# Kernel tuning notes

Hardware: AMD Instinct MI355X
Metric: run time of the kernel (lower is better)

Reference implementation:

```python
import math
import jax, jax.numpy as jnp
import numpy as np
from jax import lax

B = 4; N = 4096; F = 15; A = 24          # batch, tcr_num, feature_num, aa_num
HID = 10; H = 1; HD = 10; AFN = 14       # attn hidden, heads, head dim, sum(filter_num)
KS = [2, 3, 4, 5, 6, 7]; FN = [3, 3, 3, 2, 2, 1]
K = int(N * 0.05)                        # routing topk = 204
SCALE = np.float32(1.0 / math.sqrt(HD))


def setup_inputs() -> dict:
    key = jax.random.key(0)
    ks = jax.random.split(key, 24)
    inp = {"x": jax.random.normal(ks[0], (B, N, F, A), jnp.float32)}
    for i, (h, f) in enumerate(zip(KS, FN)):
        inp["conv_w%d" % h] = jax.random.normal(ks[1 + 2 * i], (f, F, h), jnp.float32) * 0.1
        inp["conv_b%d" % h] = jax.random.normal(ks[2 + 2 * i], (f,), jnp.float32) * 0.1
    specs = [("q", HID, AFN), ("k", HID, AFN), ("v", HID, AFN), ("attn", AFN, HID), ("mil", 2, AFN)]
    for j, (nm, o, i_) in enumerate(specs):
        inp["w_" + nm] = jax.random.normal(ks[13 + 2 * j], (o, i_), jnp.float32) * 0.1
        inp["b_" + nm] = jax.random.normal(ks[14 + 2 * j], (o,), jnp.float32) * 0.1
    return inp


def reference(x, conv_w2, conv_b2, conv_w3, conv_b3, conv_w4, conv_b4,
              conv_w5, conv_b5, conv_w6, conv_b6, conv_w7, conv_b7,
              w_q, b_q, w_k, b_k, w_v, b_v, w_attn, b_attn, w_mil, b_mil):
    # --- per-sequence conv feature extraction ---
    xc = x.reshape(-1, F, A)  # [B*N, 15, 24]
    feats = []
    for w, b in [(conv_w2, conv_b2), (conv_w3, conv_b3), (conv_w4, conv_b4),
                 (conv_w5, conv_b5), (conv_w6, conv_b6), (conv_w7, conv_b7)]:
        y = lax.conv_general_dilated(xc, w, (1,), 'VALID',
                                     dimension_numbers=('NCH', 'OIH', 'NCH'))
        y = jax.nn.relu(y + b[None, :, None])
        feats.append(jnp.max(y, axis=-1))  # AdaptiveMaxPool1d(1)
    out = jnp.concatenate(feats, axis=1).reshape(B, N, AFN)  # [B, N, 14]

    # --- QKV projections, split into heads -> [B, H, N, HD] ---
    q = (out @ w_q.T + b_q).reshape(B, N, H, HD).transpose(0, 2, 1, 3)
    k = (out @ w_k.T + b_k).reshape(B, N, H, HD).transpose(0, 2, 1, 3)
    v = (out @ w_v.T + b_v).reshape(B, N, H, HD).transpose(0, 2, 1, 3)

    # --- bi-level routing: full scores, topk over head-mean (detached in torch) ---
    scores_raw = jnp.einsum('bhnd,bhmd->bhnm', q, k)  # [B, H, N, N]
    a_r = jnp.mean(lax.stop_gradient(scores_raw), axis=1)  # [B, N, N]
    _, idx = lax.top_k(a_r, K)  # [B, N, K] int32
    idx_r = jnp.broadcast_to(idx[:, None], (B, H, N, K))

    scores = jnp.take_along_axis(scores_raw * SCALE, idx_r, axis=3)  # [B, H, N, K]
    # gather values per (batch, head, query): v_g[b,h,i,j] = v[b,h,idx[b,h,i,j]]
    v_g = jax.vmap(jax.vmap(lambda vh, ih: vh[ih]))(v, idx_r)  # [B, H, N, K, HD]

    probs = jax.nn.softmax(scores, axis=-1)  # dropout is identity at p=0 / eval
    ctx = jnp.einsum('bhnk,bhnkd->bhnd', probs, v_g)  # [B, H, N, HD]
    ctx = ctx.transpose(0, 2, 1, 3).reshape(B, N, HID)

    ctx = ctx @ w_attn.T + b_attn          # [B, N, 14]
    logits = ctx @ w_mil.T + b_mil          # [B, N, 2]
    pooled = jnp.sum(logits, axis=1) / N    # [B, 2]
    return pooled, probs[:, :, :, None, :]  # probs shaped [B, H, N, 1, K] as in torch
```

## Files before the change

### kernel.cpp

```cpp
#include <hip/hip_runtime.h>
#include <math.h>

#define NB 4
#define NN 4096
#define KSEL 204
#define NBINS 512
#define CANDN 256
#define QKSCALE 0.31622776601683794f

#define WS_Q 0
#define WS_KT (NB * NN * 10)
#define WS_V (2 * NB * NN * 10)
#define WS_LG (3 * NB * NN * 10)

#define SEQ_PER_BLOCK 16

__global__ __launch_bounds__(256) void featqkv_kernel(
    const float* __restrict__ x,
    const float* __restrict__ w2, const float* __restrict__ b2,
    const float* __restrict__ w3, const float* __restrict__ b3,
    const float* __restrict__ w4, const float* __restrict__ b4,
    const float* __restrict__ w5, const float* __restrict__ b5,
    const float* __restrict__ w6, const float* __restrict__ b6,
    const float* __restrict__ w7, const float* __restrict__ b7,
    const float* __restrict__ wq, const float* __restrict__ bq,
    const float* __restrict__ wk, const float* __restrict__ bk,
    const float* __restrict__ wv, const float* __restrict__ bv,
    float* __restrict__ q_out, float* __restrict__ kT_out, float* __restrict__ v_out)
{
    __shared__ float xs[SEQ_PER_BLOCK * 360];
    __shared__ float wconv[840];
    __shared__ float bconv[14];
    __shared__ float wqkv[420];
    __shared__ float bqkv[30];
    __shared__ float feats[SEQ_PER_BLOCK * 14];

    const int t = threadIdx.x;
    const int g0 = blockIdx.x * SEQ_PER_BLOCK;

    const float* xg = x + (size_t)g0 * 360;
    for (int i = t; i < SEQ_PER_BLOCK * 360; i += 256) xs[i] = xg[i];
    for (int i = t; i < 90; i += 256) wconv[i] = w2[i];
    for (int i = t; i < 135; i += 256) wconv[90 + i] = w3[i];
    for (int i = t; i < 180; i += 256) wconv[225 + i] = w4[i];
    for (int i = t; i < 150; i += 256) wconv[405 + i] = w5[i];
    for (int i = t; i < 180; i += 256) wconv[555 + i] = w6[i];
    for (int i = t; i < 105; i += 256) wconv[735 + i] = w7[i];
    if (t < 3) bconv[t] = b2[t];
    else if (t < 6) bconv[t] = b3[t - 3];
    else if (t < 9) bconv[t] = b4[t - 6];
    else if (t < 11) bconv[t] = b5[t - 9];
    else if (t < 13) bconv[t] = b6[t - 11];
    else if (t == 13) bconv[t] = b7[0];
    for (int i = t; i < 140; i += 256) wqkv[i] = wq[i];
    for (int i = t; i < 140; i += 256) wqkv[140 + i] = wk[i];
    for (int i = t; i < 140; i += 256) wqkv[280 + i] = wv[i];
    if (t < 10) bqkv[t] = bq[t];
    else if (t < 20) bqkv[t] = bk[t - 10];
    else if (t < 30) bqkv[t] = bv[t - 20];
    __syncthreads();

    const int seq = t >> 4;
    const int wkr = t & 15;

    if (wkr < 14) {
        const int ch = wkr;
        int h, fi, woff;
        if (ch < 3)       { h = 2; fi = ch;      woff = 0   + fi * 30; }
        else if (ch < 6)  { h = 3; fi = ch - 3;  woff = 90  + fi * 45; }
        else if (ch < 9)  { h = 4; fi = ch - 6;  woff = 225 + fi * 60; }
        else if (ch < 11) { h = 5; fi = ch - 9;  woff = 405 + fi * 75; }
        else if (ch < 13) { h = 6; fi = ch - 11; woff = 555 + fi * 90; }
        else              { h = 7; fi = 0;       woff = 735; }
        const int T = 24 - h + 1;

        float acc[23];
#pragma unroll
        for (int i2 = 0; i2 < 23; i2++) acc[i2] = 0.f;
        const float* xrow = &xs[seq * 360];
        for (int c = 0; c < 15; c++) {
            float xr[24];
#pragma unroll
            for (int u = 0; u < 24; u++) xr[u] = xrow[c * 24 + u];
#pragma unroll
            for (int j = 0; j < 7; j++) {
                if (j < h) {
                    float wv_ = wconv[woff + c * h + j];
#pragma unroll
                    for (int tt = 0; tt < 23; tt++) {
                        if (tt < T) acc[tt] = fmaf(xr[tt + j], wv_, acc[tt]);
                    }
                }
            }
        }
        float m = -1e30f;
#pragma unroll
        for (int tt = 0; tt < 23; tt++) {
            if (tt < T) m = fmaxf(m, acc[tt]);
        }
        feats[seq * 14 + ch] = fmaxf(m + bconv[ch], 0.f);
    }
    __syncthreads();

    const int g = g0 + seq;
    const int b_ = g >> 12;
    const int n_ = g & 4095;
    for (int o = wkr; o < 30; o += 16) {
        const int type = o / 10;
        const int comp = o % 10;
        const float* wrow = &wqkv[type * 140 + comp * 14];
        const float* frow = &feats[seq * 14];
        float a = bqkv[type * 10 + comp];
#pragma unroll
        for (int ii = 0; ii < 14; ii++) a = fmaf(frow[ii], wrow[ii], a);
        if (type == 0) q_out[(size_t)g * 10 + comp] = a;
        else if (type == 1) kT_out[((size_t)b_ * 10 + comp) * NN + n_] = a;
        else v_out[(size_t)g * 10 + comp] = a;
    }
}

__device__ __forceinline__ float dec_key(unsigned int k) {
    return (k & 0x80000000u) ? __uint_as_float(k ^ 0x80000000u)
                             : __uint_as_float(~k);
}
__device__ __forceinline__ unsigned int enc_key(float s) {
    unsigned int u = __float_as_uint(s);
    return (u & 0x80000000u) ? ~u : (u | 0x80000000u);
}

__global__ __launch_bounds__(256, 6) void attn_kernel(
    const float* __restrict__ qbuf, const float* __restrict__ kTbuf,
    const float* __restrict__ vbuf,
    const float* __restrict__ w_attn, const float* __restrict__ b_attn,
    const float* __restrict__ w_mil, const float* __restrict__ b_mil,
    float* __restrict__ out_probs, float* __restrict__ logits)
{
    __shared__ unsigned int base_[NBINS];
    __shared__ unsigned int bc_[NBINS];
    __shared__ unsigned long long cand[CANDN];
    __shared__ float hpart[4], lpart[4], fpart[4];
    __shared__ unsigned int wtot[4];
    __shared__ float ctxp[40];
    __shared__ float ctx_sh[10];
    __shared__ float attn_sh[14];

    const int t = threadIdx.x;
    const int lane = t & 63;
    const int w = t >> 6;
    const int row = blockIdx.x;
    const int b_ = row >> 12;

    float q0, q1, q2, q3, q4, q5, q6, q7, q8, q9;
    {
        const float* qp = qbuf + (size_t)row * 10;
        q0 = qp[0]; q1 = qp[1]; q2 = qp[2]; q3 = qp[3]; q4 = qp[4];
        q5 = qp[5]; q6 = qp[6]; q7 = qp[7]; q8 = qp[8]; q9 = qp[9];
    }
    const float* kTb = kTbuf + (size_t)b_ * 10 * NN;
    float sc[16];
    float vhi = -1e30f, vlo = 1e30f;
#pragma unroll
    for (int i = 0; i < 4; i++) {
        float4 a0 = make_float4(0.f, 0.f, 0.f, 0.f);
#pragma unroll
        for (int c = 0; c < 10; c++) {
            const float qc = (c == 0) ? q0 : (c == 1) ? q1 : (c == 2) ? q2 : (c == 3) ? q3 :
                             (c == 4) ? q4 : (c == 5) ? q5 : (c == 6) ? q6 : (c == 7) ? q7 :
                             (c == 8) ? q8 : q9;
            const float4 kv = reinterpret_cast<const float4*>(kTb + c * NN)[i * 256 + t];
            a0.x = fmaf(qc, kv.x, a0.x);
            a0.y = fmaf(qc, kv.y, a0.y);
            a0.z = fmaf(qc, kv.z, a0.z);
            a0.w = fmaf(qc, kv.w, a0.w);
        }
        sc[i * 4 + 0] = a0.x; sc[i * 4 + 1] = a0.y;
        sc[i * 4 + 2] = a0.z; sc[i * 4 + 3] = a0.w;
        vhi = fmaxf(vhi, fmaxf(fmaxf(a0.x, a0.y), fmaxf(a0.z, a0.w)));
        vlo = fminf(vlo, fminf(fminf(a0.x, a0.y), fminf(a0.z, a0.w)));
    }
#pragma unroll
    for (int off = 32; off > 0; off >>= 1) {
        vhi = fmaxf(vhi, __shfl_xor(vhi, off));
        vlo = fminf(vlo, __shfl_xor(vlo, off));
    }
    if (lane == 0) { hpart[w] = vhi; lpart[w] = vlo; }
    base_[2 * t] = 0u; base_[2 * t + 1] = 0u;
    cand[t] = 0ULL;
    __syncthreads();
    const float hi = fmaxf(fmaxf(hpart[0], hpart[1]), fmaxf(hpart[2], hpart[3]));
    const float lo = fminf(fminf(lpart[0], lpart[1]), fminf(lpart[2], lpart[3]));
    const bool degen = (hi <= lo);

    float pv = 0.f;
    int jj = 0, p = KSEL;
    bool selected = false;
    const float smax = hi * QKSCALE;

    if (!degen) {
        const float scale = (float)(NBINS - 1) / (hi - lo);

#pragma unroll
        for (int i = 0; i < 16; i++) {
            const int bin = (int)fminf((sc[i] - lo) * scale, (float)(NBINS - 1));
            atomicAdd(&base_[bin], 1u);
        }
        __syncthreads();

        {
            const unsigned int c0 = base_[2 * t];
            const unsigned int c1 = base_[2 * t + 1];
            const unsigned int T_ = c0 + c1;
            unsigned int acc = T_;
#pragma unroll
            for (int off = 1; off < 64; off <<= 1) {
                unsigned int o = __shfl_down(acc, off);
                if (lane + off < 64) acc += o;
            }
            if (lane == 0) wtot[w] = acc;
            __syncthreads();
            unsigned int tail = 0u;
#pragma unroll
            for (int w2 = 1; w2 < 4; w2++) if (w2 > w) tail += wtot[w2];
            const unsigned int A = (acc - T_) + tail;
            base_[2 * t + 1] = A;
            base_[2 * t] = A + c1;
            bc_[2 * t + 1] = A;
            bc_[2 * t] = A + c1;
        }
        __syncthreads();

#pragma unroll
        for (int i = 0; i < 16; i++) {
            const int bin = (int)fminf((sc[i] - lo) * scale, (float)(NBINS - 1));
            const unsigned int bs = base_[bin];
            if (bs < KSEL) {
                const unsigned int pos = atomicAdd(&bc_[bin], 1u);
                if (pos < CANDN) {
                    const int j = (i >> 2) * 1024 + t * 4 + (i & 3);
                    cand[pos] = (((unsigned long long)enc_key(sc[i])) << 16)
                              | (unsigned long long)(4095 - j);
                }
            }
        }
        __syncthreads();

        const unsigned long long mine = cand[t];
        if (mine != 0ULL) {
            const float s = dec_key((unsigned int)(mine >> 16));
            const int bin = (int)fminf((s - lo) * scale, (float)(NBINS - 1));
            const unsigned int bs = base_[bin];
            unsigned int end = (bin < NBINS - 1) ? 0u : 0u;
            end = (bin == NBINS - 1) ? bs + (4096u) : base_[bin + 1];
            unsigned int e2 = (bin > 0) ? base_[bin - 1] : 4096u;
            if (e2 > CANDN) e2 = CANDN;
            unsigned int rank = 0;
            for (unsigned int s2 = bs; s2 < e2; s2++)
                rank += (cand[s2] > mine) ? 1u : 0u;
            const unsigned int pp = bs + rank;
            if (pp < KSEL) {
                selected = true;
                p = (int)pp;
                jj = 4095 - (int)(mine & 0xFFFFu);
                pv = expf(s * QKSCALE - smax);
            }
        }
    } else {
        if (t < KSEL) {
            selected = true;
            p = t;
            jj = t;
            pv = 1.f;
        }
    }

    float dsum = pv;
#pragma unroll
    for (int off = 32; off > 0; off >>= 1) dsum += __shfl_xor(dsum, off);
    if (lane == 0) fpart[w] = dsum;
    __syncthreads();
    const float inv = 1.f / (fpart[0] + fpart[1] + fpart[2] + fpart[3]);

    float cx0 = 0.f, cx1 = 0.f, cx2 = 0.f, cx3 = 0.f, cx4 = 0.f;
    float cx5 = 0.f, cx6 = 0.f, cx7 = 0.f, cx8 = 0.f, cx9 = 0.f;
    if (selected) {
        const float pn = pv * inv;
        out_probs[(size_t)row * KSEL + p] = pn;
        const float* vr = vbuf + ((size_t)b_ * NN + (size_t)jj) * 10;
        const float2 v01 = reinterpret_cast<const float2*>(vr)[0];
        const float2 v23 = reinterpret_cast<const float2*>(vr)[1];
        const float2 v45 = reinterpret_cast<const float2*>(vr)[2];
        const float2 v67 = reinterpret_cast<const float2*>(vr)[3];
        const float2 v89 = reinterpret_cast<const float2*>(vr)[4];
        cx0 = pn * v01.x; cx1 = pn * v01.y;
        cx2 = pn * v23.x; cx3 = pn * v23.y;
        cx4 = pn * v45.x; cx5 = pn * v45.y;
        cx6 = pn * v67.x; cx7 = pn * v67.y;
        cx8 = pn * v89.x; cx9 = pn * v89.y;
    }
#pragma unroll
    for (int off = 32; off > 0; off >>= 1) {
        cx0 += __shfl_xor(cx0, off); cx1 += __shfl_xor(cx1, off);
        cx2 += __shfl_xor(cx2, off); cx3 += __shfl_xor(cx3, off);
        cx4 += __shfl_xor(cx4, off); cx5 += __shfl_xor(cx5, off);
        cx6 += __shfl_xor(cx6, off); cx7 += __shfl_xor(cx7, off);
        cx8 += __shfl_xor(cx8, off); cx9 += __shfl_xor(cx9, off);
    }
    if (lane == 0) {
        ctxp[w * 10 + 0] = cx0; ctxp[w * 10 + 1] = cx1; ctxp[w * 10 + 2] = cx2;
        ctxp[w * 10 + 3] = cx3; ctxp[w * 10 + 4] = cx4; ctxp[w * 10 + 5] = cx5;
        ctxp[w * 10 + 6] = cx6; ctxp[w * 10 + 7] = cx7; ctxp[w * 10 + 8] = cx8;
        ctxp[w * 10 + 9] = cx9;
    }
    __syncthreads();
    if (t < 10) ctx_sh[t] = ctxp[t] + ctxp[10 + t] + ctxp[20 + t] + ctxp[30 + t];
    __syncthreads();

    if (t < 14) {
        float a = b_attn[t];
#pragma unroll
        for (int d = 0; d < 10; d++) a = fmaf(ctx_sh[d], w_attn[t * 10 + d], a);
        attn_sh[t] = a;
    }
    __syncthreads();
    if (t < 2) {
        float lg = b_mil[t];
#pragma unroll
        for (int ii = 0; ii < 14; ii++) lg = fmaf(attn_sh[ii], w_mil[t * 14 + ii], lg);
        logits[(size_t)row * 2 + t] = lg;
    }
}

__global__ __launch_bounds__(256) void pool_kernel(
    const float* __restrict__ logits, float* __restrict__ out)
{
    __shared__ float red[256];
    const int t = threadIdx.x;
    const int bc = blockIdx.x;
    const int b_ = bc >> 1;
    const int c_ = bc & 1;
    float a = 0.f;
    for (int n2 = t; n2 < NN; n2 += 256)
        a += logits[((size_t)b_ * NN + n2) * 2 + c_];
    red[t] = a;
    __syncthreads();
    for (int off = 128; off > 0; off >>= 1) {
        if (t < off) red[t] += red[t + off];
        __syncthreads();
    }
    if (t == 0) out[bc] = red[0] * (1.f / 4096.f);
}

extern "C" void kernel_launch(void* const* d_in, const int* in_sizes, int n_in,
                              void* d_out, int out_size, void* d_ws, size_t ws_size,
                              hipStream_t stream) {
    const float* x  = (const float*)d_in[0];
    const float* w2 = (const float*)d_in[1];  const float* b2 = (const float*)d_in[2];
    const float* w3 = (const float*)d_in[3];  const float* b3 = (const float*)d_in[4];
    const float* w4 = (const float*)d_in[5];  const float* b4 = (const float*)d_in[6];
    const float* w5 = (const float*)d_in[7];  const float* b5 = (const float*)d_in[8];
    const float* w6 = (const float*)d_in[9];  const float* b6 = (const float*)d_in[10];
    const float* w7 = (const float*)d_in[11]; const float* b7 = (const float*)d_in[12];
    const float* wq = (const float*)d_in[13]; const float* bq = (const float*)d_in[14];
    const float* wk = (const float*)d_in[15]; const float* bk = (const float*)d_in[16];
    const float* wv = (const float*)d_in[17]; const float* bv = (const float*)d_in[18];
    const float* wat = (const float*)d_in[19]; const float* bat = (const float*)d_in[20];
    const float* wm = (const float*)d_in[21];  const float* bm = (const float*)d_in[22];

    float* ws = (float*)d_ws;
    float* qb = ws + WS_Q;
    float* kT = ws + WS_KT;
    float* vb = ws + WS_V;
    float* lg = ws + WS_LG;
    float* out = (float*)d_out;

    hipLaunchKernelGGL(featqkv_kernel, dim3(NB * NN / SEQ_PER_BLOCK), dim3(256), 0, stream,
                       x, w2, b2, w3, b3, w4, b4, w5, b5, w6, b6, w7, b7,
                       wq, bq, wk, bk, wv, bv, qb, kT, vb);
    hipLaunchKernelGGL(attn_kernel, dim3(NB * NN), dim3(256), 0, stream,
                       qb, kT, vb, wat, bat, wm, bm, out + 8, lg);
    hipLaunchKernelGGL(pool_kernel, dim3(8), dim3(256), 0, stream, lg, out);
}
```

Measured before the change: 260.3 us.

## Pad conv weights to uniform 7 taps, block K-transpose layout, raise occupancy

In the feature kernel, conv weights are repacked into a zero-padded 14x15x7 shared array. Every channel lane then runs the same unrolled 7-tap, 23-output loop with no h-dependent branches, and the input is loaded into shared memory and registers as float4. K-transpose is stored in 64-column tiles, so each score float4 load reads from a block-local 640-float region. The attention kernel's launch bound goes from 6 to 8 blocks per SIMD, which risks register pressure or spills, and the padding adds wasted FMAs for the short filters.

Measured after the change: 320.1 us. 1.23x slower.

```diff
diff --git a/kernel.cpp b/kernel.cpp
--- a/kernel.cpp
+++ b/kernel.cpp
@@ -14,6 +14,7 @@
 #define WS_LG (3 * NB * NN * 10)
 
 #define SEQ_PER_BLOCK 16
+
 
 __global__ __launch_bounds__(256) void featqkv_kernel(
     const float* __restrict__ x,
@@ -28,8 +29,8 @@
     const float* __restrict__ wv, const float* __restrict__ bv,
     float* __restrict__ q_out, float* __restrict__ kT_out, float* __restrict__ v_out)
 {
-    __shared__ float xs[SEQ_PER_BLOCK * 360];
-    __shared__ float wconv[840];
+    __shared__ __align__(16) float xs[SEQ_PER_BLOCK * 360];
+    __shared__ float wpad[14 * 105];
     __shared__ float bconv[14];
     __shared__ float wqkv[420];
     __shared__ float bqkv[30];
@@ -38,14 +39,26 @@
     const int t = threadIdx.x;
     const int g0 = blockIdx.x * SEQ_PER_BLOCK;
 
-    const float* xg = x + (size_t)g0 * 360;
-    for (int i = t; i < SEQ_PER_BLOCK * 360; i += 256) xs[i] = xg[i];
-    for (int i = t; i < 90; i += 256) wconv[i] = w2[i];
-    for (int i = t; i < 135; i += 256) wconv[90 + i] = w3[i];
-    for (int i = t; i < 180; i += 256) wconv[225 + i] = w4[i];
-    for (int i = t; i < 150; i += 256) wconv[405 + i] = w5[i];
-    for (int i = t; i < 180; i += 256) wconv[555 + i] = w6[i];
-    for (int i = t; i < 105; i += 256) wconv[735 + i] = w7[i];
+    {
+        const float4* xg4 = reinterpret_cast<const float4*>(x + (size_t)g0 * 360);
+        float4* xs4 = reinterpret_cast<float4*>(xs);
+        for (int i = t; i < SEQ_PER_BLOCK * 90; i += 256) xs4[i] = xg4[i];
+    }
+
+    for (int i = t; i < 14 * 105; i += 256) {
+        const int ch = i / 105;
+        const int r = i - ch * 105;
+        const int c = r / 7;
+        const int j = r - (r / 7) * 7;
+        float val = 0.f;
+        if (ch < 3)       { if (j < 2) val = w2[ch * 30 + c * 2 + j]; }
+        else if (ch < 6)  { if (j < 3) val = w3[(ch - 3) * 45 + c * 3 + j]; }
+        else if (ch < 9)  { if (j < 4) val = w4[(ch - 6) * 60 + c * 4 + j]; }
+        else if (ch < 11) { if (j < 5) val = w5[(ch - 9) * 75 + c * 5 + j]; }
+        else if (ch < 13) { if (j < 6) val = w6[(ch - 11) * 90 + c * 6 + j]; }
+        else              { val = w7[c * 7 + j]; }
+        wpad[i] = val;
+    }
     if (t < 3) bconv[t] = b2[t];
     else if (t < 6) bconv[t] = b3[t - 3];
     else if (t < 9) bconv[t] = b4[t - 6];
@@ -65,39 +78,38 @@
 
     if (wkr < 14) {
         const int ch = wkr;
-        int h, fi, woff;
-        if (ch < 3)       { h = 2; fi = ch;      woff = 0   + fi * 30; }
-        else if (ch < 6)  { h = 3; fi = ch - 3;  woff = 90  + fi * 45; }
-        else if (ch < 9)  { h = 4; fi = ch - 6;  woff = 225 + fi * 60; }
-        else if (ch < 11) { h = 5; fi = ch - 9;  woff = 405 + fi * 75; }
-        else if (ch < 13) { h = 6; fi = ch - 11; woff = 555 + fi * 90; }
-        else              { h = 7; fi = 0;       woff = 735; }
-        const int T = 24 - h + 1;
+        int T;
+        if (ch < 3) T = 23; else if (ch < 6) T = 22; else if (ch < 9) T = 21;
+        else if (ch < 11) T = 20; else if (ch < 13) T = 19; else T = 18;
 
         float acc[23];
 #pragma unroll
-        for (int i2 = 0; i2 < 23; i2++) acc[i2] = 0.f;
+        for (int u = 0; u < 23; u++) acc[u] = 0.f;
         const float* xrow = &xs[seq * 360];
+        const float* wrow = &wpad[ch * 105];
         for (int c = 0; c < 15; c++) {
-            float xr[24];
-#pragma unroll
-            for (int u = 0; u < 24; u++) xr[u] = xrow[c * 24 + u];
+            float xr[30];
+            const float4* xp = reinterpret_cast<const float4*>(xrow + c * 24);
+#pragma unroll
+            for (int u4 = 0; u4 < 6; u4++) {
+                const float4 xv = xp[u4];
+                xr[u4 * 4 + 0] = xv.x; xr[u4 * 4 + 1] = xv.y;
+                xr[u4 * 4 + 2] = xv.z; xr[u4 * 4 + 3] = xv.w;
+            }
+#pragma unroll
+            for (int u = 24; u < 30; u++) xr[u] = 0.f;
 #pragma unroll
             for (int j = 0; j < 7; j++) {
-                if (j < h) {
-                    float wv_ = wconv[woff + c * h + j];
-#pragma unroll
-                    for (int tt = 0; tt < 23; tt++) {
-                        if (tt < T) acc[tt] = fmaf(xr[tt + j], wv_, acc[tt]);
-                    }
-                }
-            }
-        }
-        float m = -1e30f;
-#pragma unroll
-        for (int tt = 0; tt < 23; tt++) {
+                const float wv_ = wrow[c * 7 + j];
+#pragma unroll
+                for (int tt = 0; tt < 23; tt++)
+                    acc[tt] = fmaf(xr[tt + j], wv_, acc[tt]);
+            }
+        }
+        float m = -3.0e38f;
+#pragma unroll
+        for (int tt = 0; tt < 23; tt++)
             if (tt < T) m = fmaxf(m, acc[tt]);
-        }
         feats[seq * 14 + ch] = fmaxf(m + bconv[ch], 0.f);
     }
     __syncthreads();
@@ -114,7 +126,8 @@
 #pragma unroll
         for (int ii = 0; ii < 14; ii++) a = fmaf(frow[ii], wrow[ii], a);
         if (type == 0) q_out[(size_t)g * 10 + comp] = a;
-        else if (type == 1) kT_out[((size_t)b_ * 10 + comp) * NN + n_] = a;
+        else if (type == 1)
+            kT_out[(size_t)b_ * 40960 + (size_t)(n_ >> 6) * 640 + comp * 64 + (n_ & 63)] = a;
         else v_out[(size_t)g * 10 + comp] = a;
     }
 }
@@ -128,7 +141,7 @@
     return (u & 0x80000000u) ? ~u : (u | 0x80000000u);
 }
 
-__global__ __launch_bounds__(256, 6) void attn_kernel(
+__global__ __launch_bounds__(256, 8) void attn_kernel(
     const float* __restrict__ qbuf, const float* __restrict__ kTbuf,
     const float* __restrict__ vbuf,
     const float* __restrict__ w_attn, const float* __restrict__ b_attn,
@@ -150,33 +163,32 @@
     const int row = blockIdx.x;
     const int b_ = row >> 12;
 
-    float q0, q1, q2, q3, q4, q5, q6, q7, q8, q9;
+    float qr[10];
     {
         const float* qp = qbuf + (size_t)row * 10;
-        q0 = qp[0]; q1 = qp[1]; q2 = qp[2]; q3 = qp[3]; q4 = qp[4];
-        q5 = qp[5]; q6 = qp[6]; q7 = qp[7]; q8 = qp[8]; q9 = qp[9];
-    }
-    const float* kTb = kTbuf + (size_t)b_ * 10 * NN;
+#pragma unroll
+        for (int c = 0; c < 10; c++) qr[c] = qp[c];
+    }
+    const float* kTb = kTbuf + (size_t)b_ * 40960;
     float sc[16];
     float vhi = -1e30f, vlo = 1e30f;
 #pragma unroll
     for (int i = 0; i < 4; i++) {
-        float4 a0 = make_float4(0.f, 0.f, 0.f, 0.f);
+        const float4* kp = reinterpret_cast<const float4*>(
+            kTb + (size_t)(i * 16 + (t >> 4)) * 640 + (t & 15) * 4);
+        float ax = 0.f, ay = 0.f, az = 0.f, aw = 0.f;
 #pragma unroll
         for (int c = 0; c < 10; c++) {
-            const float qc = (c == 0) ? q0 : (c == 1) ? q1 : (c == 2) ? q2 : (c == 3) ? q3 :
-                             (c == 4) ? q4 : (c == 5) ? q5 : (c == 6) ? q6 : (c == 7) ? q7 :
-                             (c == 8) ? q8 : q9;
-            const float4 kv = reinterpret_cast<const float4*>(kTb + c * NN)[i * 256 + t];
-            a0.x = fmaf(qc, kv.x, a0.x);
-            a0.y = fmaf(qc, kv.y, a0.y);
-            a0.z = fmaf(qc, kv.z, a0.z);
-            a0.w = fmaf(qc, kv.w, a0.w);
-        }
-        sc[i * 4 + 0] = a0.x; sc[i * 4 + 1] = a0.y;
-        sc[i * 4 + 2] = a0.z; sc[i * 4 + 3] = a0.w;
-        vhi = fmaxf(vhi, fmaxf(fmaxf(a0.x, a0.y), fmaxf(a0.z, a0.w)));
-        vlo = fminf(vlo, fminf(fminf(a0.x, a0.y), fminf(a0.z, a0.w)));
+            const float4 kv = kp[c * 16];
+            ax = fmaf(qr[c], kv.x, ax);
+            ay = fmaf(qr[c], kv.y, ay);
+            az = fmaf(qr[c], kv.z, az);
+            aw = fmaf(qr[c], kv.w, aw);
+        }
+        sc[i * 4 + 0] = ax; sc[i * 4 + 1] = ay;
+        sc[i * 4 + 2] = az; sc[i * 4 + 3] = aw;
+        vhi = fmaxf(vhi, fmaxf(fmaxf(ax, ay), fmaxf(az, aw)));
+        vlo = fminf(vlo, fminf(fminf(ax, ay), fminf(az, aw)));
     }
 #pragma unroll
     for (int off = 32; off > 0; off >>= 1) {
@@ -249,8 +261,6 @@
             const float s = dec_key((unsigned int)(mine >> 16));
             const int bin = (int)fminf((s - lo) * scale, (float)(NBINS - 1));
             const unsigned int bs = base_[bin];
-            unsigned int end = (bin < NBINS - 1) ? 0u : 0u;
-            end = (bin == NBINS - 1) ? bs + (4096u) : base_[bin + 1];
             unsigned int e2 = (bin > 0) ? base_[bin - 1] : 4096u;
             if (e2 > CANDN) e2 = CANDN;
             unsigned int rank = 0;
```
